# Kernel optimization log

Hardware: AMD Instinct MI355X
Metric: run time of the kernel (lower is better)

The kernel has to match this reference:

```python
import jax, jax.numpy as jnp
import numpy as np

B, S, D = 2, 2048, 1024
H = 16
HD = D // H
MLP = 4096
EPS = 1e-6


def _layernorm(x, g, b):
    mu = jnp.mean(x, axis=-1, keepdims=True)
    var = jnp.var(x, axis=-1, keepdims=True)
    return (x - mu) * jax.lax.rsqrt(var + EPS) * g + b


def setup_inputs() -> dict:
    key = jax.random.key(0)
    ks = jax.random.split(key, 16)
    sd = 1.0 / np.sqrt(D)
    sm = 1.0 / np.sqrt(MLP)
    return {
        "x": jax.random.normal(ks[0], (B, S, D), jnp.float32),
        "ln1_g": jnp.ones((D,), jnp.float32),
        "ln1_b": jnp.zeros((D,), jnp.float32),
        "wq": jax.random.normal(ks[1], (D, D), jnp.float32) * sd,
        "bq": jnp.zeros((D,), jnp.float32),
        "wk": jax.random.normal(ks[2], (D, D), jnp.float32) * sd,
        "bk": jnp.zeros((D,), jnp.float32),
        "wv": jax.random.normal(ks[3], (D, D), jnp.float32) * sd,
        "bv": jnp.zeros((D,), jnp.float32),
        "wo": jax.random.normal(ks[4], (D, D), jnp.float32) * sd,
        "bo": jnp.zeros((D,), jnp.float32),
        "ln2_g": jnp.ones((D,), jnp.float32),
        "ln2_b": jnp.zeros((D,), jnp.float32),
        "w1": jax.random.normal(ks[5], (D, MLP), jnp.float32) * sd,
        "b1": jnp.zeros((MLP,), jnp.float32),
        "w2": jax.random.normal(ks[6], (MLP, D), jnp.float32) * sm,
        "b2": jnp.zeros((D,), jnp.float32),
    }


def reference(x, ln1_g, ln1_b, wq, bq, wk, bk, wv, bv, wo, bo,
              ln2_g, ln2_b, w1, b1, w2, b2):
    # --- attention sub-block (pre-LN) ---
    h = _layernorm(x, ln1_g, ln1_b)
    q = (h @ wq + bq).reshape(B, S, H, HD).transpose(0, 2, 1, 3)  # [B,H,S,HD]
    k = (h @ wk + bk).reshape(B, S, H, HD).transpose(0, 2, 1, 3)
    v = (h @ wv + bv).reshape(B, S, H, HD).transpose(0, 2, 1, 3)
    scale = HD ** -0.5
    attn = jax.nn.softmax(jnp.einsum('bhqd,bhkd->bhqk', q, k) * scale, axis=-1)
    out = jnp.einsum('bhqk,bhkd->bhqd', attn, v)
    out = out.transpose(0, 2, 1, 3).reshape(B, S, D)
    x = x + (out @ wo + bo)
    # --- MLP sub-block (pre-LN) ---
    h = _layernorm(x, ln2_g, ln2_b)
    h = jax.nn.gelu(h @ w1 + b1, approximate=False)
    x = x + (h @ w2 + b2)
    return x
```

## Files before the change

### kernel.cpp

```cpp
#include <hip/hip_runtime.h>
#include <hip/hip_bf16.h>

typedef unsigned short u16;
typedef unsigned int u32;
typedef __attribute__((ext_vector_type(8))) unsigned short us8;
typedef __attribute__((ext_vector_type(4))) unsigned short us4;
typedef __attribute__((ext_vector_type(2))) unsigned int u32x2;
typedef __attribute__((ext_vector_type(8))) short bf16x8;
typedef __attribute__((ext_vector_type(4))) float f32x4;

#define QSCALE 0.18033688011112042f

__device__ __forceinline__ u16 f2bf(float f) {
    __hip_bfloat16 h = __float2bfloat16(f);
    return __builtin_bit_cast(u16, h);
}
__device__ __forceinline__ u32 cvtpk(float lo, float hi) {
    u32 r;
    asm("v_cvt_pk_bf16_f32 %0, %1, %2" : "=v"(r) : "v"(lo), "v"(hi));
    return r;
}
__device__ __forceinline__ void gll16(const u16* g, u16* l) {
    __builtin_amdgcn_global_load_lds(
        (const __attribute__((address_space(1))) unsigned int*)g,
        (__attribute__((address_space(3))) unsigned int*)l, 16, 0, 0);
}

__global__ void tcvt_k(const float* __restrict__ W, u16* __restrict__ Wt, int KK, int NN)
{
    __shared__ float tile[32][33];
    const int n0 = blockIdx.x * 32, k0 = blockIdx.y * 32;
    const int tx = threadIdx.x, ty = threadIdx.y;
    #pragma unroll
    for (int j = ty; j < 32; j += 8)
        tile[j][tx] = W[(size_t)(k0 + j) * NN + n0 + tx];
    __syncthreads();
    #pragma unroll
    for (int j = ty; j < 32; j += 8)
        Wt[(size_t)(n0 + j) * KK + k0 + tx] = f2bf(tile[tx][j]);
}

__global__ void tcvt4_k(const float* __restrict__ a, const float* __restrict__ b,
                        const float* __restrict__ c, const float* __restrict__ d,
                        u16* __restrict__ out)
{
    __shared__ float tile[32][33];
    const int z = blockIdx.z;
    const float* W = (z == 0) ? a : (z == 1) ? b : (z == 2) ? c : d;
    u16* Wt = out + (size_t)z * 1024 * 1024;
    const int n0 = blockIdx.x * 32, k0 = blockIdx.y * 32;
    const int tx = threadIdx.x, ty = threadIdx.y;
    #pragma unroll
    for (int j = ty; j < 32; j += 8)
        tile[j][tx] = W[(size_t)(k0 + j) * 1024 + n0 + tx];
    __syncthreads();
    #pragma unroll
    for (int j = ty; j < 32; j += 8)
        Wt[(size_t)(n0 + j) * 1024 + k0 + tx] = f2bf(tile[tx][j]);
}

__global__ __launch_bounds__(256) void vtr_k(const u16* __restrict__ Vb, u16* __restrict__ Vt)
{
    __shared__ u16 t[64][72];
    const int bh = blockIdx.y, s0 = blockIdx.x * 64;
    const int tid = threadIdx.x;
    const size_t ibase = (size_t)bh * 2048 * 64 + (size_t)s0 * 64;
    #pragma unroll
    for (int c = tid; c < 512; c += 256) {
        const us8 v = *(const us8*)(Vb + ibase + (size_t)(c >> 3) * 64 + (c & 7) * 8);
        *(us8*)(&t[c >> 3][(c & 7) * 8]) = v;
    }
    __syncthreads();
    const size_t obase = (size_t)bh * 64 * 2048 + s0;
    #pragma unroll
    for (int c = tid; c < 512; c += 256) {
        const int hd = c >> 3, sl0 = (c & 7) * 8;
        us8 v;
        #pragma unroll
        for (int j = 0; j < 8; j++) v[j] = t[sl0 + j][hd];
        *(us8*)(Vt + obase + (size_t)hd * 2048 + sl0) = v;
    }
}

__global__ __launch_bounds__(256) void ln_k(const float* __restrict__ x,
                                            const float* __restrict__ g,
                                            const float* __restrict__ b,
                                            u16* __restrict__ h)
{
    __shared__ float red[8];
    const int row = blockIdx.x;
    const int tid = threadIdx.x;
    const float4 v = *(const float4*)(x + (size_t)row * 1024 + tid * 4);
    float sum = v.x + v.y + v.z + v.w;
    float sq  = v.x * v.x + v.y * v.y + v.z * v.z + v.w * v.w;
    #pragma unroll
    for (int off = 32; off >= 1; off >>= 1) {
        sum += __shfl_down(sum, off);
        sq  += __shfl_down(sq, off);
    }
    const int l = tid & 63, w = tid >> 6;
    if (l == 0) { red[w * 2] = sum; red[w * 2 + 1] = sq; }
    __syncthreads();
    sum = red[0] + red[2] + red[4] + red[6];
    sq  = red[1] + red[3] + red[5] + red[7];
    const float mean = sum * (1.0f / 1024.0f);
    const float var  = sq * (1.0f / 1024.0f) - mean * mean;
    const float inv  = rsqrtf(var + 1e-6f);
    const int c = tid * 4;
    us4 out;
    out[0] = f2bf((v.x - mean) * inv * g[c + 0] + b[c + 0]);
    out[1] = f2bf((v.y - mean) * inv * g[c + 1] + b[c + 1]);
    out[2] = f2bf((v.z - mean) * inv * g[c + 2] + b[c + 2]);
    out[3] = f2bf((v.w - mean) * inv * g[c + 3] + b[c + 3]);
    *(us4*)(h + (size_t)row * 1024 + c) = out;
}

template<int EPI, int TM, int BK>
__device__ __forceinline__ void gemm_body(const u16* __restrict__ A,
                                          const u16* __restrict__ Bt,
                                          const float* __restrict__ bias,
                                          void* __restrict__ outp,
                                          const float* __restrict__ addsrc,
                                          int K, float scale, int m0, int n0)
{
    constexpr int MI  = TM / 32;
    constexpr int ASZ = TM * BK;
    constexpr int BSZ = 128 * BK;
    constexpr int RPI = 512 / BK;
    constexpr int NIA = (TM / 4) / RPI;
    constexpr int NIB = 32 / RPI;
    constexpr int NI  = NIA + NIB;
    __shared__ u16 As[2 * ASZ];
    __shared__ u16 Bs[2 * BSZ];
    const int tid = threadIdx.x;
    const int l = tid & 63, w = tid >> 6;
    const int wr = w >> 1, wc = w & 1;
    const int lr = l & 15, lg = l >> 4;

    int srow, sblk;
    if constexpr (BK == 32) { srow = l >> 2; sblk = (l & 3) ^ ((l >> 3) & 3); }
    else                    { srow = l >> 3; sblk = (l & 7) ^ (l >> 3); }
    const u16* gA = A  + (size_t)(m0 + w * (TM / 4) + srow) * K + sblk * 8;
    const u16* gB = Bt + (size_t)(n0 + w * 32 + srow) * K + sblk * 8;
    const size_t rowKi = (size_t)RPI * K;
    u16* const lA0 = As + w * (TM / 4) * BK;
    u16* const lB0 = Bs + w * 32 * BK;

    f32x4 acc[MI][4];
    #pragma unroll
    for (int i = 0; i < MI; i++)
        #pragma unroll
        for (int j = 0; j < 4; j++) acc[i][j] = (f32x4)(0.0f);

    auto stage = [&](int buf, int kb) {
        u16* la = lA0 + buf * ASZ;
        u16* lb = lB0 + buf * BSZ;
        #pragma unroll
        for (int i = 0; i < NIA; i++) gll16(gA + kb + i * rowKi, la + i * 512);
        #pragma unroll
        for (int i = 0; i < NIB; i++) gll16(gB + kb + i * rowKi, lb + i * 512);
    };

    const int nK = K / BK;
    stage(0, 0);
    int cur = 0;
    for (int kt = 0; kt < nK; ++kt) {
        __builtin_amdgcn_sched_barrier(0);
        __builtin_amdgcn_s_barrier();
        __builtin_amdgcn_sched_barrier(0);
        if (kt + 1 < nK) {
            stage(cur ^ 1, (kt + 1) * BK);
            if constexpr (NI == 4)      asm volatile("s_waitcnt vmcnt(4)" ::: "memory");
            else if constexpr (NI == 6) asm volatile("s_waitcnt vmcnt(6)" ::: "memory");
            else                        asm volatile("s_waitcnt vmcnt(8)" ::: "memory");
        } else {
            asm volatile("s_waitcnt vmcnt(0)" ::: "memory");
        }
        __builtin_amdgcn_s_barrier();
        __builtin_amdgcn_sched_barrier(0);

        const u16* as = As + cur * ASZ;
        const u16* bs = Bs + cur * BSZ;
        #pragma unroll
        for (int ks = 0; ks < BK / 32; ks++) {
            int off;
            if constexpr (BK == 32) off = (lg ^ ((lr >> 1) & 3)) * 8;
            else                    off = ((ks * 4 + lg) ^ (lr & 7)) * 8;
            bf16x8 af[MI], bf[4];
            #pragma unroll
            for (int mi = 0; mi < MI; mi++)
                af[mi] = *(const bf16x8*)(as + (wr * (MI * 16) + mi * 16 + lr) * BK + off);
            #pragma unroll
            for (int ni = 0; ni < 4; ni++)
                bf[ni] = *(const bf16x8*)(bs + (wc * 64 + ni * 16 + lr) * BK + off);
            #pragma unroll
            for (int mi = 0; mi < MI; mi++)
                #pragma unroll
                for (int ni = 0; ni < 4; ni++)
                    acc[mi][ni] = __builtin_amdgcn_mfma_f32_16x16x32_bf16(
                        af[mi], bf[ni], acc[mi][ni], 0, 0, 0);
        }
        cur ^= 1;
    }

    const int r0 = lg * 4;
    #pragma unroll
    for (int mi = 0; mi < MI; mi++) {
        #pragma unroll
        for (int ni = 0; ni < 4; ni++) {
            const int col = n0 + wc * 64 + ni * 16 + lr;
            const float bv = bias[col];
            #pragma unroll
            for (int r = 0; r < 4; r++) {
                const int row = m0 + wr * (MI * 16) + mi * 16 + r0 + r;
                const float v = acc[mi][ni][r] + bv;
                if constexpr (EPI == 0) {
                    const int bb = row >> 11, s = row & 2047;
                    const int hh = col >> 6, hd = col & 63;
                    ((u16*)outp)[(((size_t)(bb * 16 + hh) * 2048) + s) * 64 + hd] = f2bf(v * scale);
                } else if constexpr (EPI == 1 || EPI == 3) {
                    const size_t idx = (size_t)row * 1024 + col;
                    ((float*)outp)[idx] = addsrc[idx] + v;
                } else {
                    const float gl = 0.5f * v * (1.0f + erff(v * 0.70710678118654752f));
                    ((u16*)outp)[(size_t)row * 4096 + col] = f2bf(gl);
                }
            }
        }
    }
}

template<int EPI, int TM, int BK, int NX>
__global__ __launch_bounds__(256) void gemm_k(const u16* __restrict__ A,
                                              const u16* __restrict__ Bt,
                                              const float* __restrict__ bias,
                                              void* __restrict__ outp,
                                              const float* __restrict__ addsrc,
                                              int K)
{
    const int nwg = gridDim.x;
    const int s = (blockIdx.x & 7) * (nwg >> 3) + (blockIdx.x >> 3);
    gemm_body<EPI, TM, BK>(A, Bt, bias, outp, addsrc, K, 1.0f,
                           (s / NX) * TM, (s % NX) * 128);
}

__global__ __launch_bounds__(256) void gemm_qkv_k(const u16* __restrict__ A,
                                                  const u16* __restrict__ WtBase,
                                                  const float* __restrict__ bq,
                                                  const float* __restrict__ bk,
                                                  const float* __restrict__ bv,
                                                  u16* __restrict__ outBase)
{
    const int s = (blockIdx.x & 7) * 96 + (blockIdx.x >> 3);
    const int z = s >> 8, r = s & 255;
    const u16* Bt = WtBase + (size_t)z * 1024 * 1024;
    const float* bias = (z == 0) ? bq : (z == 1) ? bk : bv;
    u16* outp = outBase + (size_t)z * 4096 * 1024;
    const float scale = (z == 0) ? QSCALE : 1.0f;
    gemm_body<0, 128, 32>(A, Bt, bias, outp, nullptr, 1024, scale,
                          (r >> 3) * 128, (r & 7) * 128);
}

__global__ __launch_bounds__(256) void attn_mfma_k(
    const u16* __restrict__ Qb, const u16* __restrict__ Kb,
    const u16* __restrict__ Vt, u16* __restrict__ Oo)
{
    __shared__ u16 Kl[2][64 * 64];
    __shared__ u16 Vl[2][64 * 64];
    __shared__ u16 Pl[4][16 * 64];

    const int tid = threadIdx.x;
    const int l = tid & 63, w = tid >> 6;
    const int lr = l & 15, lg = l >> 4;
    const int bid = blockIdx.x;
    const int bh = (bid & 7) * 4 + ((bid >> 3) >> 5);
    const int qblk = (bid >> 3) & 31;
    const size_t base = (size_t)bh * 2048 * 64;
    const int q0 = qblk * 64 + w * 16;

    bf16x8 qf[2];
    #pragma unroll
    for (int ks = 0; ks < 2; ks++)
        qf[ks] = *(const bf16x8*)(Qb + base + (size_t)(q0 + lr) * 64 + ks * 32 + lg * 8);

    bf16x8 onef;
    #pragma unroll
    for (int j = 0; j < 8; j++) onef[j] = (short)0x3F80;

    f32x4 o_[4];
    f32x4 ol;
    #pragma unroll
    for (int r = 0; r < 4; r++) {
        ol[r] = 0.0f;
        #pragma unroll
        for (int ni = 0; ni < 4; ni++) o_[ni][r] = 0.0f;
    }

    u16* const plw = &Pl[w][0];
    u16* pw_[4];
    #pragma unroll
    for (int ni = 0; ni < 4; ni++)
        pw_[ni] = plw + lr * 64 + (((ni * 2 + (lg >> 1)) ^ (lr & 7)) * 8 + (lg & 1) * 4);
    const u16* const pr0 = plw + lr * 64 + ((lg ^ (lr & 7)) * 8);
    const u16* const pr1 = plw + lr * 64 + (((4 + lg) ^ (lr & 7)) * 8);

    const int srow = w * 16 + (l >> 3);
    const int sblk = (l & 7) ^ (l >> 3);
    const u16* gK = Kb + base + (size_t)srow * 64 + sblk * 8;
    const u16* gV = Vt + (size_t)bh * 64 * 2048 + (size_t)srow * 2048 + sblk * 8;
    u16* const kd = &Kl[0][0] + w * 1024;
    u16* const vd = &Vl[0][0] + w * 1024;

    auto stageT = [&](int buf, int kv) {
        u16* kdb = kd + buf * 4096;
        u16* vdb = vd + buf * 4096;
        gll16(gK + (size_t)kv * 64, kdb);
        gll16(gK + (size_t)kv * 64 + 512, kdb + 512);
        gll16(gV + kv, vdb);
        gll16(gV + kv + 8 * 2048, vdb + 512);
    };

    stageT(0, 0);
    int cur = 0;
    for (int t = 0; t < 32; ++t) {
        __builtin_amdgcn_sched_barrier(0);
        __builtin_amdgcn_s_barrier();
        __builtin_amdgcn_sched_barrier(0);
        if (t < 31) {
            stageT(cur ^ 1, (t + 1) * 64);
            asm volatile("s_waitcnt vmcnt(4)" ::: "memory");
        } else {
            asm volatile("s_waitcnt vmcnt(0)" ::: "memory");
        }
        __builtin_amdgcn_s_barrier();
        __builtin_amdgcn_sched_barrier(0);

        f32x4 s_[4];
        #pragma unroll
        for (int ni = 0; ni < 4; ni++) s_[ni] = (f32x4)(0.0f);
        __builtin_amdgcn_s_setprio(1);
        #pragma unroll
        for (int ks = 0; ks < 2; ks++)
            #pragma unroll
            for (int ni = 0; ni < 4; ni++) {
                const int row = ni * 16 + lr;
                const bf16x8 kf = *(const bf16x8*)(
                    &Kl[cur][row * 64 + (((ks * 4 + lg) ^ (row & 7)) * 8)]);
                s_[ni] = __builtin_amdgcn_mfma_f32_16x16x32_bf16(kf, qf[ks], s_[ni], 0, 0, 0);
            }
        __builtin_amdgcn_s_setprio(0);

        #pragma unroll
        for (int ni = 0; ni < 4; ni++) {
            u32x2 pv;
            pv[0] = cvtpk(exp2f(s_[ni][0]), exp2f(s_[ni][1]));
            pv[1] = cvtpk(exp2f(s_[ni][2]), exp2f(s_[ni][3]));
            *(u32x2*)pw_[ni] = pv;
        }

        __builtin_amdgcn_s_setprio(1);
        #pragma unroll
        for (int ks = 0; ks < 2; ks++) {
            const bf16x8 pf = *(const bf16x8*)(ks ? pr1 : pr0);
            ol = __builtin_amdgcn_mfma_f32_16x16x32_bf16(pf, onef, ol, 0, 0, 0);
            #pragma unroll
            for (int ni = 0; ni < 4; ni++) {
                const int row = ni * 16 + lr;
                const bf16x8 vf = *(const bf16x8*)(
                    &Vl[cur][row * 64 + (((ks * 4 + lg) ^ (row & 7)) * 8)]);
                o_[ni] = __builtin_amdgcn_mfma_f32_16x16x32_bf16(pf, vf, o_[ni], 0, 0, 0);
            }
        }
        __builtin_amdgcn_s_setprio(0);
        cur ^= 1;
    }

    const int bb = bh >> 4, hh = bh & 15;
    #pragma unroll
    for (int r = 0; r < 4; r++) {
        const float inv = 1.0f / ol[r];
        const int qrow = q0 + lg * 4 + r;
        u16* dst = Oo + ((size_t)(bb * 2048 + qrow)) * 1024 + hh * 64;
        #pragma unroll
        for (int ni = 0; ni < 4; ni++)
            dst[ni * 16 + lr] = f2bf(o_[ni][r] * inv);
    }
}

extern "C" void kernel_launch(void* const* d_in, const int* in_sizes, int n_in,
                              void* d_out, int out_size, void* d_ws, size_t ws_size,
                              hipStream_t stream)
{
    const float* x     = (const float*)d_in[0];
    const float* ln1_g = (const float*)d_in[1];
    const float* ln1_b = (const float*)d_in[2];
    const float* wq    = (const float*)d_in[3];
    const float* bq    = (const float*)d_in[4];
    const float* wk    = (const float*)d_in[5];
    const float* bk    = (const float*)d_in[6];
    const float* wv    = (const float*)d_in[7];
    const float* bv    = (const float*)d_in[8];
    const float* wo    = (const float*)d_in[9];
    const float* bo    = (const float*)d_in[10];
    const float* ln2_g = (const float*)d_in[11];
    const float* ln2_b = (const float*)d_in[12];
    const float* w1    = (const float*)d_in[13];
    const float* b1    = (const float*)d_in[14];
    const float* w2    = (const float*)d_in[15];
    const float* b2    = (const float*)d_in[16];

    char* ws = (char*)d_ws;
    size_t off = 0;
    auto alloc = [&](size_t bytes) {
        char* p = ws + off;
        off += (bytes + 255) & ~(size_t)255;
        return p;
    };
    u16* wtq = (u16*)alloc((size_t)1024 * 1024 * 2);
    u16* wtk = (u16*)alloc((size_t)1024 * 1024 * 2);
    u16* wtv = (u16*)alloc((size_t)1024 * 1024 * 2);
    u16* wto = (u16*)alloc((size_t)1024 * 1024 * 2);
    u16* wt1 = (u16*)alloc((size_t)4096 * 1024 * 2);
    u16* wt2 = (u16*)alloc((size_t)1024 * 4096 * 2);
    u16* h1  = (u16*)alloc((size_t)4096 * 1024 * 2);
    u16* qb  = (u16*)alloc((size_t)4096 * 1024 * 2);
    u16* kb  = (u16*)alloc((size_t)4096 * 1024 * 2);
    u16* vb  = (u16*)alloc((size_t)4096 * 1024 * 2);
    u16* ao  = (u16*)alloc((size_t)4096 * 1024 * 2);
    float* x2 = (float*)alloc((size_t)4096 * 1024 * 4);
    u16* h2  = (u16*)alloc((size_t)4096 * 1024 * 2);
    u16* mid = (u16*)alloc((size_t)4096 * 4096 * 2);
    u16* vt  = mid;
    (void)ws_size;
    (void)wtk; (void)wtv;

    const dim3 tb(32, 8);
    tcvt4_k<<<dim3(32, 32, 4), tb, 0, stream>>>(wq, wk, wv, wo, wtq);
    tcvt_k<<<dim3(128, 32), tb, 0, stream>>>(w1, wt1, 1024, 4096);
    tcvt_k<<<dim3(32, 128), tb, 0, stream>>>(w2, wt2, 4096, 1024);

    ln_k<<<4096, 256, 0, stream>>>(x, ln1_g, ln1_b, h1);

    gemm_qkv_k<<<768, 256, 0, stream>>>(h1, wtq, bq, bk, bv, qb);

    vtr_k<<<dim3(32, 32), 256, 0, stream>>>(vb, vt);
    attn_mfma_k<<<1024, 256, 0, stream>>>(qb, kb, vt, ao);

    gemm_k<1, 64, 64, 8><<<512, 256, 0, stream>>>(ao, wto, bo, x2, x, 1024);

    ln_k<<<4096, 256, 0, stream>>>(x2, ln2_g, ln2_b, h2);

    gemm_k<2, 64, 64, 32><<<2048, 256, 0, stream>>>(h2, wt1, b1, mid, nullptr, 1024);
    gemm_k<3, 64, 64, 8><<<512, 256, 0, stream>>>(mid, wt2, b2, (float*)d_out, x2, 4096);
}
```

Measured before the change: 271.3 us.

## Process two 16-row query groups per wave in attention to reuse K/V tiles

Each attention wave now handles 32 query rows (two 16-row groups) instead of 16, so every K and V fragment read from LDS feeds two MFMAs and each block covers 128 queries; the grid is halved to 512 blocks. This amortizes the K/V global-to-LDS staging and LDS reads over twice the compute. exp2f is also replaced by the raw hardware exp2 builtin. The cost is more accumulator registers, twice the P scratch in LDS, and fewer blocks for the 256 CUs, which may lower occupancy and parallelism.

```diff
diff --git a/kernel.cpp b/kernel.cpp
--- a/kernel.cpp
+++ b/kernel.cpp
@@ -19,6 +19,9 @@
     u32 r;
     asm("v_cvt_pk_bf16_f32 %0, %1, %2" : "=v"(r) : "v"(lo), "v"(hi));
     return r;
+}
+__device__ __forceinline__ float ex2(float x) {
+    return __builtin_amdgcn_exp2f(x);
 }
 __device__ __forceinline__ void gll16(const u16* g, u16* l) {
     __builtin_amdgcn_global_load_lds(
@@ -267,42 +270,51 @@
 {
     __shared__ u16 Kl[2][64 * 64];
     __shared__ u16 Vl[2][64 * 64];
-    __shared__ u16 Pl[4][16 * 64];
+    __shared__ u16 Pl[4][32 * 64];
 
     const int tid = threadIdx.x;
     const int l = tid & 63, w = tid >> 6;
     const int lr = l & 15, lg = l >> 4;
     const int bid = blockIdx.x;
-    const int bh = (bid & 7) * 4 + ((bid >> 3) >> 5);
-    const int qblk = (bid >> 3) & 31;
+    const int bh = (bid & 7) * 4 + ((bid >> 3) >> 4);
+    const int qblk = (bid >> 3) & 15;
     const size_t base = (size_t)bh * 2048 * 64;
-    const int q0 = qblk * 64 + w * 16;
-
-    bf16x8 qf[2];
-    #pragma unroll
-    for (int ks = 0; ks < 2; ks++)
-        qf[ks] = *(const bf16x8*)(Qb + base + (size_t)(q0 + lr) * 64 + ks * 32 + lg * 8);
+    const int q0 = qblk * 128 + w * 32;
+
+    bf16x8 qf[2][2];
+    #pragma unroll
+    for (int g = 0; g < 2; g++)
+        #pragma unroll
+        for (int ks = 0; ks < 2; ks++)
+            qf[g][ks] = *(const bf16x8*)(Qb + base + (size_t)(q0 + g * 16 + lr) * 64
+                                         + ks * 32 + lg * 8);
 
     bf16x8 onef;
     #pragma unroll
     for (int j = 0; j < 8; j++) onef[j] = (short)0x3F80;
 
-    f32x4 o_[4];
-    f32x4 ol;
-    #pragma unroll
-    for (int r = 0; r < 4; r++) {
-        ol[r] = 0.0f;
-        #pragma unroll
-        for (int ni = 0; ni < 4; ni++) o_[ni][r] = 0.0f;
+    f32x4 o_[2][4];
+    f32x4 ol[2];
+    #pragma unroll
+    for (int g = 0; g < 2; g++) {
+        #pragma unroll
+        for (int r = 0; r < 4; r++) ol[g][r] = 0.0f;
+        #pragma unroll
+        for (int ni = 0; ni < 4; ni++) o_[g][ni] = (f32x4)(0.0f);
     }
 
     u16* const plw = &Pl[w][0];
-    u16* pw_[4];
-    #pragma unroll
-    for (int ni = 0; ni < 4; ni++)
-        pw_[ni] = plw + lr * 64 + (((ni * 2 + (lg >> 1)) ^ (lr & 7)) * 8 + (lg & 1) * 4);
-    const u16* const pr0 = plw + lr * 64 + ((lg ^ (lr & 7)) * 8);
-    const u16* const pr1 = plw + lr * 64 + (((4 + lg) ^ (lr & 7)) * 8);
+    u16* pw_[2][4];
+    const u16* pr_[2][2];
+    #pragma unroll
+    for (int g = 0; g < 2; g++) {
+        #pragma unroll
+        for (int ni = 0; ni < 4; ni++)
+            pw_[g][ni] = plw + (g * 16 + lr) * 64
+                       + (((ni * 2 + (lg >> 1)) ^ (lr & 7)) * 8 + (lg & 1) * 4);
+        pr_[g][0] = plw + (g * 16 + lr) * 64 + ((lg ^ (lr & 7)) * 8);
+        pr_[g][1] = plw + (g * 16 + lr) * 64 + (((4 + lg) ^ (lr & 7)) * 8);
+    }
 
     const int srow = w * 16 + (l >> 3);
     const int sblk = (l & 7) ^ (l >> 3);
@@ -335,9 +347,11 @@
         __builtin_amdgcn_s_barrier();
         __builtin_amdgcn_sched_barrier(0);
 
-        f32x4 s_[4];
-        #pragma unroll
-        for (int ni = 0; ni < 4; ni++) s_[ni] = (f32x4)(0.0f);
+        f32x4 s_[2][4];
+        #pragma unroll
+        for (int g = 0; g < 2; g++)
+            #pragma unroll
+            for (int ni = 0; ni < 4; ni++) s_[g][ni] = (f32x4)(0.0f);
         __builtin_amdgcn_s_setprio(1);
         #pragma unroll
         for (int ks = 0; ks < 2; ks++)
@@ -346,29 +360,35 @@
                 const int row = ni * 16 + lr;
                 const bf16x8 kf = *(const bf16x8*)(
                     &Kl[cur][row * 64 + (((ks * 4 + lg) ^ (row & 7)) * 8)]);
-                s_[ni] = __builtin_amdgcn_mfma_f32_16x16x32_bf16(kf, qf[ks], s_[ni], 0, 0, 0);
+                s_[0][ni] = __builtin_amdgcn_mfma_f32_16x16x32_bf16(kf, qf[0][ks], s_[0][ni], 0, 0, 0);
+                s_[1][ni] = __builtin_amdgcn_mfma_f32_16x16x32_bf16(kf, qf[1][ks], s_[1][ni], 0, 0, 0);
             }
         __builtin_amdgcn_s_setprio(0);
 
         #pragma unroll
-        for (int ni = 0; ni < 4; ni++) {
-            u32x2 pv;
-            pv[0] = cvtpk(exp2f(s_[ni][0]), exp2f(s_[ni][1]));
-            pv[1] = cvtpk(exp2f(s_[ni][2]), exp2f(s_[ni][3]));
-            *(u32x2*)pw_[ni] = pv;
-        }
+        for (int g = 0; g < 2; g++)
+            #pragma unroll
+            for (int ni = 0; ni < 4; ni++) {
+                u32x2 pv;
+                pv[0] = cvtpk(ex2(s_[g][ni][0]), ex2(s_[g][ni][1]));
+                pv[1] = cvtpk(ex2(s_[g][ni][2]), ex2(s_[g][ni][3]));
+                *(u32x2*)pw_[g][ni] = pv;
+            }
 
         __builtin_amdgcn_s_setprio(1);
         #pragma unroll
         for (int ks = 0; ks < 2; ks++) {
-            const bf16x8 pf = *(const bf16x8*)(ks ? pr1 : pr0);
-            ol = __builtin_amdgcn_mfma_f32_16x16x32_bf16(pf, onef, ol, 0, 0, 0);
+            const bf16x8 pf0 = *(const bf16x8*)pr_[0][ks];
+            const bf16x8 pf1 = *(const bf16x8*)pr_[1][ks];
+            ol[0] = __builtin_amdgcn_mfma_f32_16x16x32_bf16(pf0, onef, ol[0], 0, 0, 0);
+            ol[1] = __builtin_amdgcn_mfma_f32_16x16x32_bf16(pf1, onef, ol[1], 0, 0, 0);
             #pragma unroll
             for (int ni = 0; ni < 4; ni++) {
                 const int row = ni * 16 + lr;
                 const bf16x8 vf = *(const bf16x8*)(
                     &Vl[cur][row * 64 + (((ks * 4 + lg) ^ (row & 7)) * 8)]);
-                o_[ni] = __builtin_amdgcn_mfma_f32_16x16x32_bf16(pf, vf, o_[ni], 0, 0, 0);
+                o_[0][ni] = __builtin_amdgcn_mfma_f32_16x16x32_bf16(pf0, vf, o_[0][ni], 0, 0, 0);
+                o_[1][ni] = __builtin_amdgcn_mfma_f32_16x16x32_bf16(pf1, vf, o_[1][ni], 0, 0, 0);
             }
         }
         __builtin_amdgcn_s_setprio(0);
@@ -377,14 +397,16 @@
 
     const int bb = bh >> 4, hh = bh & 15;
     #pragma unroll
-    for (int r = 0; r < 4; r++) {
-        const float inv = 1.0f / ol[r];
-        const int qrow = q0 + lg * 4 + r;
-        u16* dst = Oo + ((size_t)(bb * 2048 + qrow)) * 1024 + hh * 64;
-        #pragma unroll
-        for (int ni = 0; ni < 4; ni++)
-            dst[ni * 16 + lr] = f2bf(o_[ni][r] * inv);
-    }
+    for (int g = 0; g < 2; g++)
+        #pragma unroll
+        for (int r = 0; r < 4; r++) {
+            const float inv = 1.0f / ol[g][r];
+            const int qrow = q0 + g * 16 + lg * 4 + r;
+            u16* dst = Oo + ((size_t)(bb * 2048 + qrow)) * 1024 + hh * 64;
+            #pragma unroll
+            for (int ni = 0; ni < 4; ni++)
+                dst[ni * 16 + lr] = f2bf(o_[g][ni][r] * inv);
+        }
 }
 
 extern "C" void kernel_launch(void* const* d_in, const int* in_sizes, int n_in,
@@ -444,7 +466,7 @@
     gemm_qkv_k<<<768, 256, 0, stream>>>(h1, wtq, bq, bk, bv, qb);
 
     vtr_k<<<dim3(32, 32), 256, 0, stream>>>(vb, vt);
-    attn_mfma_k<<<1024, 256, 0, stream>>>(qb, kb, vt, ao);
+    attn_mfma_k<<<512, 256, 0, stream>>>(qb, kb, vt, ao);
 
     gemm_k<1, 64, 64, 8><<<512, 256, 0, stream>>>(ao, wto, bo, x2, x, 1024);
 
```

Result: faster. 255.1 us (-6.0%).
